# Kernel tuning notes

Hardware: AMD Instinct MI355X
Metric: run time of the kernel (lower is better)

## Reference

```python
import jax, jax.numpy as jnp
import numpy as np

N = 100000   # nodes
E = 1600000  # directed edges (avg degree 16)
IN, HID, OUT = 32, 64, 32


def setup_inputs() -> dict:
    key = jax.random.key(0)
    k0, k1, k2, k3 = jax.random.split(key, 4)
    x = jax.random.normal(k0, (N, IN), dtype=jnp.float32)
    edge_index = jax.random.randint(k1, (2, E), 0, N, dtype=jnp.int32)
    W1 = jax.random.normal(k2, (IN, HID), dtype=jnp.float32) * (1.0 / np.sqrt(IN))
    b1 = jnp.zeros((HID,), dtype=jnp.float32)
    W2 = jax.random.normal(k3, (HID, OUT), dtype=jnp.float32) * (1.0 / np.sqrt(HID))
    b2 = jnp.zeros((OUT,), dtype=jnp.float32)
    return {"x": x, "edge_index": edge_index, "W1": W1, "b1": b1, "W2": W2, "b2": b2}


def gcn_conv(x, src, dst, W, b, n):
    # GCNConv: D^{-1/2} (A + I) D^{-1/2} X W + b, deg computed after self-loops
    h = x @ W                                   # [N, d_out]
    ones = jnp.ones_like(dst, dtype=h.dtype)
    deg = jax.ops.segment_sum(ones, dst, num_segments=n)   # >= 1 (self-loops)
    dinv = jax.lax.rsqrt(jnp.maximum(deg, 1.0))
    norm = dinv[src] * dinv[dst]                # [E + N]
    agg = jax.ops.segment_sum(norm[:, None] * h[src], dst, num_segments=n)
    return agg + b


def reference(x, edge_index, W1, b1, W2, b2):
    n = x.shape[0]
    loop = jnp.arange(n, dtype=edge_index.dtype)
    src = jnp.concatenate([edge_index[0], loop])  # add self-loops once
    dst = jnp.concatenate([edge_index[1], loop])
    h = jax.nn.relu(gcn_conv(x, src, dst, W1, b1, n))
    # dropout omitted (eval mode)
    out = gcn_conv(h, src, dst, W2, b2, n)
    return out
```

## Files before the change

kernel.cpp:

```cpp
#include <hip/hip_runtime.h>
#include <stdint.h>

#define IN_F  32
#define HID_F 64
#define OUT_F 32

#define BKT_SHIFT 8
#define BKT_NODES 256
#define NBLK      512

__device__ inline unsigned short f2bf(float f) {
    unsigned u = __float_as_uint(f);
    return (unsigned short)((u + 0x7FFF + ((u >> 16) & 1)) >> 16);
}
__device__ inline float bflo(unsigned w) { return __uint_as_float(w << 16); }
__device__ inline float bfhi(unsigned w) { return __uint_as_float(w & 0xFFFF0000u); }

__global__ __launch_bounds__(256) void count_kernel(const int* __restrict__ dst,
                                                    int* __restrict__ cnt, int E, int nb)
{
    __shared__ int hist[1024];
    int tid = threadIdx.x;
    for (int i = tid; i < nb; i += 256) hist[i] = 0;
    __syncthreads();
    for (int e = blockIdx.x * 256 + tid; e < E; e += NBLK * 256)
        atomicAdd(&hist[dst[e] >> BKT_SHIFT], 1);
    __syncthreads();
    for (int i = tid; i < nb; i += 256) cnt[i * NBLK + blockIdx.x] = hist[i];
}

__global__ __launch_bounds__(NBLK) void bsum_kernel(const int* __restrict__ cnt,
                                                    int* __restrict__ bsum)
{
    __shared__ int s[NBLK];
    int tid = threadIdx.x, b = blockIdx.x;
    s[tid] = cnt[b * NBLK + tid];
    __syncthreads();
    for (int off = NBLK / 2; off > 0; off >>= 1) {
        if (tid < off) s[tid] += s[tid + off];
        __syncthreads();
    }
    if (tid == 0) bsum[b] = s[0];
}

__global__ __launch_bounds__(512) void bscan_kernel(int* __restrict__ bsum, int nb,
                                                    int* __restrict__ cellstart, int nc,
                                                    int* __restrict__ rowstart, int n, int E)
{
    __shared__ int s[512];
    int tid = threadIdx.x;
    int my = (tid < nb) ? bsum[tid] : 0;
    s[tid] = my;
    __syncthreads();
    for (int off = 1; off < 512; off <<= 1) {
        int t = (tid >= off) ? s[tid - off] : 0;
        __syncthreads();
        s[tid] += t;
        __syncthreads();
    }
    if (tid < nb) bsum[tid] = s[tid] - my;
    if (tid == 0) { cellstart[nc] = E; rowstart[n] = E; }
}

__global__ __launch_bounds__(NBLK) void cscan_kernel(const int* __restrict__ cnt,
                                                     const int* __restrict__ bsum,
                                                     int* __restrict__ cellstart)
{
    __shared__ int s[NBLK];
    int tid = threadIdx.x, b = blockIdx.x;
    int my = cnt[b * NBLK + tid];
    s[tid] = my;
    __syncthreads();
    for (int off = 1; off < NBLK; off <<= 1) {
        int t = (tid >= off) ? s[tid - off] : 0;
        __syncthreads();
        s[tid] += t;
        __syncthreads();
    }
    cellstart[b * NBLK + tid] = bsum[b] + s[tid] - my;
}

__global__ __launch_bounds__(256) void append_kernel(
    const int* __restrict__ src, const int* __restrict__ dst,
    const int* __restrict__ cellstart, unsigned* __restrict__ pairs, int E, int nb)
{
    __shared__ int cur[1024];
    int tid = threadIdx.x;
    for (int i = tid; i < nb; i += 256) cur[i] = cellstart[i * NBLK + blockIdx.x];
    __syncthreads();
    for (int e = blockIdx.x * 256 + tid; e < E; e += NBLK * 256) {
        int d = dst[e];
        int pos = atomicAdd(&cur[d >> BKT_SHIFT], 1);
        pairs[pos] = ((unsigned)src[e] << BKT_SHIFT) | (unsigned)(d & (BKT_NODES - 1));
    }
}

__global__ __launch_bounds__(256) void place_kernel(
    const int* __restrict__ cellstart, const unsigned* __restrict__ pairs,
    int* __restrict__ srcs, int* __restrict__ rowstart, float* __restrict__ dinv, int n)
{
    __shared__ int hist[BKT_NODES];
    __shared__ int ofs[BKT_NODES];
    int b = blockIdx.x, tid = threadIdx.x;
    int beg = cellstart[b * NBLK], end = cellstart[(b + 1) * NBLK];
    hist[tid] = 0;
    __syncthreads();
    for (int e = beg + tid; e < end; e += 256)
        atomicAdd(&hist[pairs[e] & (BKT_NODES - 1)], 1);
    __syncthreads();
    int my = hist[tid];
    ofs[tid] = my;
    __syncthreads();
    for (int off = 1; off < 256; off <<= 1) {
        int t = (tid >= off) ? ofs[tid - off] : 0;
        __syncthreads();
        ofs[tid] += t;
        __syncthreads();
    }
    int excl = ofs[tid] - my;
    int node = b * BKT_NODES + tid;
    if (node < n) {
        rowstart[node] = beg + excl;
        dinv[node] = rsqrtf((float)(my + 1));
    }
    __syncthreads();
    ofs[tid] = excl;
    __syncthreads();
    for (int e = beg + tid; e < end; e += 256) {
        unsigned p = pairs[e];
        int dl = p & (BKT_NODES - 1);
        int pos = beg + atomicAdd(&ofs[dl], 1);
        srcs[pos] = (int)(p >> BKT_SHIFT);
    }
}

__global__ void xs_kernel(const float* __restrict__ x, const float* __restrict__ dinv,
                          unsigned short* __restrict__ xsb, int n) {
    int t = blockIdx.x * blockDim.x + threadIdx.x;
    if (t < n * (IN_F / 4)) {
        float d = dinv[t >> 3];
        float4 v = ((const float4*)x)[t];
        ushort4 o;
        o.x = f2bf(v.x * d); o.y = f2bf(v.y * d);
        o.z = f2bf(v.z * d); o.w = f2bf(v.w * d);
        ((ushort4*)xsb)[t] = o;
    }
}

__global__ __launch_bounds__(512) void fused1_kernel(
    const int* __restrict__ rowstart, const int* __restrict__ srcs,
    const unsigned* __restrict__ xs2, const float* __restrict__ dinv,
    const float* __restrict__ b1, const float* __restrict__ W1,
    const float* __restrict__ W2, unsigned* __restrict__ hs2p, int n)
{
    __shared__ float W1s[IN_F * HID_F];
    __shared__ float W2s[HID_F * OUT_F];
    __shared__ float grow[32][IN_F + 1];
    __shared__ float hrow[32][HID_F + 1];
    int tid = threadIdx.x;
    for (int t = tid; t < IN_F * HID_F; t += 512) W1s[t] = W1[t];
    for (int t = tid; t < HID_F * OUT_F; t += 512) W2s[t] = W2[t];

    int nl = tid >> 4;
    unsigned q = tid & 15;
    int node = blockIdx.x * 32 + nl;
    bool active = node < n;
    int nodec = active ? node : 0;

    int beg = rowstart[nodec], end = active ? rowstart[nodec + 1] : beg;
    unsigned ws = active ? xs2[((unsigned)nodec << 4) + q] : 0u;
    float a0l = bflo(ws), a0h = bfhi(ws);
    float a1l = 0.f, a1h = 0.f, a2l = 0.f, a2h = 0.f, a3l = 0.f, a3h = 0.f;
    float a4l = 0.f, a4h = 0.f, a5l = 0.f, a5h = 0.f, a6l = 0.f, a6h = 0.f;
    float a7l = 0.f, a7h = 0.f;
    int e = beg;
    for (; e + 8 <= end; e += 8) {
        unsigned o0 = ((unsigned)srcs[e]     << 4) + q, o1 = ((unsigned)srcs[e + 1] << 4) + q;
        unsigned o2 = ((unsigned)srcs[e + 2] << 4) + q, o3 = ((unsigned)srcs[e + 3] << 4) + q;
        unsigned o4 = ((unsigned)srcs[e + 4] << 4) + q, o5 = ((unsigned)srcs[e + 5] << 4) + q;
        unsigned o6 = ((unsigned)srcs[e + 6] << 4) + q, o7 = ((unsigned)srcs[e + 7] << 4) + q;
        unsigned w0 = xs2[o0], w1 = xs2[o1], w2 = xs2[o2], w3 = xs2[o3];
        unsigned w4 = xs2[o4], w5 = xs2[o5], w6 = xs2[o6], w7 = xs2[o7];
        a0l += bflo(w0); a0h += bfhi(w0); a1l += bflo(w1); a1h += bfhi(w1);
        a2l += bflo(w2); a2h += bfhi(w2); a3l += bflo(w3); a3h += bfhi(w3);
        a4l += bflo(w4); a4h += bfhi(w4); a5l += bflo(w5); a5h += bfhi(w5);
        a6l += bflo(w6); a6h += bfhi(w6); a7l += bflo(w7); a7h += bfhi(w7);
    }
    for (; e + 4 <= end; e += 4) {
        unsigned o0 = ((unsigned)srcs[e]     << 4) + q, o1 = ((unsigned)srcs[e + 1] << 4) + q;
        unsigned o2 = ((unsigned)srcs[e + 2] << 4) + q, o3 = ((unsigned)srcs[e + 3] << 4) + q;
        unsigned w0 = xs2[o0], w1 = xs2[o1], w2 = xs2[o2], w3 = xs2[o3];
        a0l += bflo(w0); a0h += bfhi(w0); a1l += bflo(w1); a1h += bfhi(w1);
        a2l += bflo(w2); a2h += bfhi(w2); a3l += bflo(w3); a3h += bfhi(w3);
    }
    for (; e < end; ++e) {
        unsigned w0 = xs2[((unsigned)srcs[e] << 4) + q];
        a0l += bflo(w0); a0h += bfhi(w0);
    }
    float dv = dinv[nodec];
    grow[nl][2 * q]     = dv * (((a0l + a1l) + (a2l + a3l)) + ((a4l + a5l) + (a6l + a7l)));
    grow[nl][2 * q + 1] = dv * (((a0h + a1h) + (a2h + a3h)) + ((a4h + a5h) + (a6h + a7h)));
    __syncthreads();

    float h0 = b1[q], h1 = b1[q + 16], h2 = b1[q + 32], h3 = b1[q + 48];
    #pragma unroll
    for (int k = 0; k < IN_F; ++k) {
        float gk = grow[nl][k];
        h0 += gk * W1s[k * HID_F + q];
        h1 += gk * W1s[k * HID_F + q + 16];
        h2 += gk * W1s[k * HID_F + q + 32];
        h3 += gk * W1s[k * HID_F + q + 48];
    }
    hrow[nl][q]      = fmaxf(h0, 0.f);
    hrow[nl][q + 16] = fmaxf(h1, 0.f);
    hrow[nl][q + 32] = fmaxf(h2, 0.f);
    hrow[nl][q + 48] = fmaxf(h3, 0.f);
    __syncthreads();

    float p0 = 0.f, p1 = 0.f;
    #pragma unroll
    for (int k = 0; k < HID_F; ++k) {
        float hk = hrow[nl][k];
        p0 += hk * W2s[k * OUT_F + 2 * q];
        p1 += hk * W2s[k * OUT_F + 2 * q + 1];
    }
    if (active) {
        unsigned pack = (unsigned)f2bf(dv * p0) | ((unsigned)f2bf(dv * p1) << 16);
        hs2p[((unsigned)node << 4) + q] = pack;
    }
}

__global__ __launch_bounds__(256) void agg2_kernel(
    const int* __restrict__ rowstart, const int* __restrict__ srcs,
    const uint2* __restrict__ hs2p2, const float* __restrict__ dinv,
    const float* __restrict__ b2, float* __restrict__ out, int n)
{
    int t = blockIdx.x * blockDim.x + threadIdx.x;
    int node = t >> 3;
    if (node >= n) return;
    unsigned r = t & 7;
    int beg = rowstart[node], end = rowstart[node + 1];
    uint2 ws = hs2p2[((unsigned)node << 3) + r];
    float a0x = bflo(ws.x), a0y = bfhi(ws.x), a0z = bflo(ws.y), a0w = bfhi(ws.y);
    float a1x = 0.f, a1y = 0.f, a1z = 0.f, a1w = 0.f;
    float a2x = 0.f, a2y = 0.f, a2z = 0.f, a2w = 0.f;
    float a3x = 0.f, a3y = 0.f, a3z = 0.f, a3w = 0.f;
    int e = beg;
    for (; e + 4 <= end; e += 4) {
        unsigned o0 = ((unsigned)srcs[e]     << 3) + r, o1 = ((unsigned)srcs[e + 1] << 3) + r;
        unsigned o2 = ((unsigned)srcs[e + 2] << 3) + r, o3 = ((unsigned)srcs[e + 3] << 3) + r;
        uint2 w0 = hs2p2[o0], w1 = hs2p2[o1], w2 = hs2p2[o2], w3 = hs2p2[o3];
        a0x += bflo(w0.x); a0y += bfhi(w0.x); a0z += bflo(w0.y); a0w += bfhi(w0.y);
        a1x += bflo(w1.x); a1y += bfhi(w1.x); a1z += bflo(w1.y); a1w += bfhi(w1.y);
        a2x += bflo(w2.x); a2y += bfhi(w2.x); a2z += bflo(w2.y); a2w += bfhi(w2.y);
        a3x += bflo(w3.x); a3y += bfhi(w3.x); a3z += bflo(w3.y); a3w += bfhi(w3.y);
    }
    for (; e < end; ++e) {
        uint2 w0 = hs2p2[((unsigned)srcs[e] << 3) + r];
        a0x += bflo(w0.x); a0y += bfhi(w0.x); a0z += bflo(w0.y); a0w += bfhi(w0.y);
    }
    float dvv = dinv[node];
    float4 bb = ((const float4*)b2)[r];
    float4 res;
    res.x = dvv * ((a0x + a1x) + (a2x + a3x)) + bb.x;
    res.y = dvv * ((a0y + a1y) + (a2y + a3y)) + bb.y;
    res.z = dvv * ((a0z + a1z) + (a2z + a3z)) + bb.z;
    res.w = dvv * ((a0w + a1w) + (a2w + a3w)) + bb.w;
    ((float4*)out)[((size_t)node << 3) + r] = res;
}

extern "C" void kernel_launch(void* const* d_in, const int* in_sizes, int n_in,
                              void* d_out, int out_size, void* d_ws, size_t ws_size,
                              hipStream_t stream) {
    const float* x  = (const float*)d_in[0];
    const int*   ei = (const int*)  d_in[1];
    const float* W1 = (const float*)d_in[2];
    const float* b1 = (const float*)d_in[3];
    const float* W2 = (const float*)d_in[4];
    const float* b2 = (const float*)d_in[5];
    float* out = (float*)d_out;

    const int n = in_sizes[0] / IN_F;
    const int E = in_sizes[1] / 2;
    const int* src = ei;
    const int* dst = ei + E;

    const int nb = (n + BKT_NODES - 1) >> BKT_SHIFT;
    const int nc = nb * NBLK;

    auto align16 = [](int* p) { return (int*)(((uintptr_t)p + 15) & ~(uintptr_t)15); };
    int* ip = (int*)d_ws;
    int* cnt       = ip;                 ip += nc;
    int* cellstart = ip;                 ip += nc + 1;
    int* bsum      = ip;                 ip += nb + 1;
    int* rowstart  = ip;                 ip += n + 1;
    ip = align16(ip);
    unsigned* pairs = (unsigned*)ip;     ip += E;
    int* srcs_srt  = ip;                 ip += E;
    float* dinv = (float*)ip;            ip += n;
    ip = align16(ip);
    unsigned* xs2  = (unsigned*)ip;      ip += (size_t)n * IN_F / 2;
    ip = align16(ip);
    unsigned* hs2p = (unsigned*)ip;

    count_kernel<<<NBLK, 256, 0, stream>>>(dst, cnt, E, nb);
    bsum_kernel <<<nb, NBLK, 0, stream>>>(cnt, bsum);
    bscan_kernel<<<1, 512, 0, stream>>>(bsum, nb, cellstart, nc, rowstart, n, E);
    cscan_kernel<<<nb, NBLK, 0, stream>>>(cnt, bsum, cellstart);
    append_kernel<<<NBLK, 256, 0, stream>>>(src, dst, cellstart, pairs, E, nb);
    place_kernel<<<nb, 256, 0, stream>>>(cellstart, pairs, srcs_srt, rowstart, dinv, n);

    xs_kernel<<<((size_t)n * 8 + 255) / 256, 256, 0, stream>>>(x, dinv, (unsigned short*)xs2, n);

    fused1_kernel<<<(n + 31) / 32, 512, 0, stream>>>(rowstart, srcs_srt, xs2, dinv, b1, W1, W2, hs2p, n);
    agg2_kernel<<<((size_t)n * 8 + 255) / 256, 256, 0, stream>>>(rowstart, srcs_srt, (const uint2*)hs2p, dinv, b2, out, n);
}
```

Baseline: 214.5 us.

## Fuse bucket-sum into count and x scaling into place; add nontemporal loads and unrolling

Drops the bsum reduction kernel and instead has count_kernel accumulate per-bucket totals atomically after a memset. The x-scaling/bf16 pack kernel is folded into place_kernel, using per-bucket dinv held in shared memory. Streaming index reads and writes now use nontemporal loads and stores, and the gather loops in both aggregation kernels get a deeper unroll to keep more loads in flight. Together these remove two launches and make the edge-index streams bypass cache residency, in exchange for global atomics and more register pressure.

```diff
diff --git a/kernel.cpp b/kernel.cpp
--- a/kernel.cpp
+++ b/kernel.cpp
@@ -16,31 +16,25 @@
 __device__ inline float bflo(unsigned w) { return __uint_as_float(w << 16); }
 __device__ inline float bfhi(unsigned w) { return __uint_as_float(w & 0xFFFF0000u); }
 
+__device__ inline int ntld(const int* p) { return __builtin_nontemporal_load(p); }
+__device__ inline unsigned ntldu(const unsigned* p) { return __builtin_nontemporal_load(p); }
+
 __global__ __launch_bounds__(256) void count_kernel(const int* __restrict__ dst,
-                                                    int* __restrict__ cnt, int E, int nb)
+                                                    int* __restrict__ cnt,
+                                                    int* __restrict__ bsum, int E, int nb)
 {
     __shared__ int hist[1024];
     int tid = threadIdx.x;
     for (int i = tid; i < nb; i += 256) hist[i] = 0;
     __syncthreads();
     for (int e = blockIdx.x * 256 + tid; e < E; e += NBLK * 256)
-        atomicAdd(&hist[dst[e] >> BKT_SHIFT], 1);
-    __syncthreads();
-    for (int i = tid; i < nb; i += 256) cnt[i * NBLK + blockIdx.x] = hist[i];
-}
-
-__global__ __launch_bounds__(NBLK) void bsum_kernel(const int* __restrict__ cnt,
-                                                    int* __restrict__ bsum)
-{
-    __shared__ int s[NBLK];
-    int tid = threadIdx.x, b = blockIdx.x;
-    s[tid] = cnt[b * NBLK + tid];
-    __syncthreads();
-    for (int off = NBLK / 2; off > 0; off >>= 1) {
-        if (tid < off) s[tid] += s[tid + off];
-        __syncthreads();
-    }
-    if (tid == 0) bsum[b] = s[0];
+        atomicAdd(&hist[ntld(&dst[e]) >> BKT_SHIFT], 1);
+    __syncthreads();
+    for (int i = tid; i < nb; i += 256) {
+        int h = hist[i];
+        cnt[i * NBLK + blockIdx.x] = h;
+        if (h) atomicAdd(&bsum[i], h);
+    }
 }
 
 __global__ __launch_bounds__(512) void bscan_kernel(int* __restrict__ bsum, int nb,
@@ -89,24 +83,28 @@
     for (int i = tid; i < nb; i += 256) cur[i] = cellstart[i * NBLK + blockIdx.x];
     __syncthreads();
     for (int e = blockIdx.x * 256 + tid; e < E; e += NBLK * 256) {
-        int d = dst[e];
+        int d = ntld(&dst[e]);
+        int s = ntld(&src[e]);
         int pos = atomicAdd(&cur[d >> BKT_SHIFT], 1);
-        pairs[pos] = ((unsigned)src[e] << BKT_SHIFT) | (unsigned)(d & (BKT_NODES - 1));
+        __builtin_nontemporal_store(((unsigned)s << BKT_SHIFT) | (unsigned)(d & (BKT_NODES - 1)),
+                                    &pairs[pos]);
     }
 }
 
 __global__ __launch_bounds__(256) void place_kernel(
     const int* __restrict__ cellstart, const unsigned* __restrict__ pairs,
-    int* __restrict__ srcs, int* __restrict__ rowstart, float* __restrict__ dinv, int n)
+    int* __restrict__ srcs, int* __restrict__ rowstart, float* __restrict__ dinv,
+    const float* __restrict__ x, unsigned* __restrict__ xs2, int n)
 {
     __shared__ int hist[BKT_NODES];
     __shared__ int ofs[BKT_NODES];
+    __shared__ float sdv[BKT_NODES];
     int b = blockIdx.x, tid = threadIdx.x;
     int beg = cellstart[b * NBLK], end = cellstart[(b + 1) * NBLK];
     hist[tid] = 0;
     __syncthreads();
     for (int e = beg + tid; e < end; e += 256)
-        atomicAdd(&hist[pairs[e] & (BKT_NODES - 1)], 1);
+        atomicAdd(&hist[ntldu(&pairs[e]) & (BKT_NODES - 1)], 1);
     __syncthreads();
     int my = hist[tid];
     ofs[tid] = my;
@@ -119,31 +117,32 @@
     }
     int excl = ofs[tid] - my;
     int node = b * BKT_NODES + tid;
+    float dv = rsqrtf((float)(my + 1));
+    sdv[tid] = dv;
     if (node < n) {
         rowstart[node] = beg + excl;
-        dinv[node] = rsqrtf((float)(my + 1));
+        dinv[node] = dv;
     }
     __syncthreads();
     ofs[tid] = excl;
     __syncthreads();
     for (int e = beg + tid; e < end; e += 256) {
-        unsigned p = pairs[e];
+        unsigned p = ntldu(&pairs[e]);
         int dl = p & (BKT_NODES - 1);
         int pos = beg + atomicAdd(&ofs[dl], 1);
         srcs[pos] = (int)(p >> BKT_SHIFT);
     }
-}
-
-__global__ void xs_kernel(const float* __restrict__ x, const float* __restrict__ dinv,
-                          unsigned short* __restrict__ xsb, int n) {
-    int t = blockIdx.x * blockDim.x + threadIdx.x;
-    if (t < n * (IN_F / 4)) {
-        float d = dinv[t >> 3];
-        float4 v = ((const float4*)x)[t];
-        ushort4 o;
-        o.x = f2bf(v.x * d); o.y = f2bf(v.y * d);
-        o.z = f2bf(v.z * d); o.w = f2bf(v.w * d);
-        ((ushort4*)xsb)[t] = o;
+    int base = b * BKT_NODES;
+    for (int idx = tid; idx < BKT_NODES * (IN_F / 2); idx += 256) {
+        int nl = idx >> 4;
+        int p  = idx & 15;
+        int nd = base + nl;
+        if (nd < n) {
+            float2 v = ((const float2*)x)[((size_t)nd << 4) + p];
+            float d = sdv[nl];
+            unsigned pack = (unsigned)f2bf(v.x * d) | ((unsigned)f2bf(v.y * d) << 16);
+            xs2[((size_t)nd << 4) + p] = pack;
+        }
     }
 }
 
@@ -174,11 +173,33 @@
     float a4l = 0.f, a4h = 0.f, a5l = 0.f, a5h = 0.f, a6l = 0.f, a6h = 0.f;
     float a7l = 0.f, a7h = 0.f;
     int e = beg;
+    for (; e + 16 <= end; e += 16) {
+        unsigned o0 = ((unsigned)ntld(&srcs[e])      << 4) + q, o1 = ((unsigned)ntld(&srcs[e + 1]) << 4) + q;
+        unsigned o2 = ((unsigned)ntld(&srcs[e + 2])  << 4) + q, o3 = ((unsigned)ntld(&srcs[e + 3]) << 4) + q;
+        unsigned o4 = ((unsigned)ntld(&srcs[e + 4])  << 4) + q, o5 = ((unsigned)ntld(&srcs[e + 5]) << 4) + q;
+        unsigned o6 = ((unsigned)ntld(&srcs[e + 6])  << 4) + q, o7 = ((unsigned)ntld(&srcs[e + 7]) << 4) + q;
+        unsigned o8 = ((unsigned)ntld(&srcs[e + 8])  << 4) + q, o9 = ((unsigned)ntld(&srcs[e + 9]) << 4) + q;
+        unsigned oa = ((unsigned)ntld(&srcs[e + 10]) << 4) + q, ob = ((unsigned)ntld(&srcs[e + 11]) << 4) + q;
+        unsigned oc = ((unsigned)ntld(&srcs[e + 12]) << 4) + q, od = ((unsigned)ntld(&srcs[e + 13]) << 4) + q;
+        unsigned oe = ((unsigned)ntld(&srcs[e + 14]) << 4) + q, of_ = ((unsigned)ntld(&srcs[e + 15]) << 4) + q;
+        unsigned w0 = xs2[o0], w1 = xs2[o1], w2 = xs2[o2], w3 = xs2[o3];
+        unsigned w4 = xs2[o4], w5 = xs2[o5], w6 = xs2[o6], w7 = xs2[o7];
+        unsigned w8 = xs2[o8], w9 = xs2[o9], wa = xs2[oa], wb = xs2[ob];
+        unsigned wc = xs2[oc], wd = xs2[od], we = xs2[oe], wf = xs2[of_];
+        a0l += bflo(w0); a0h += bfhi(w0); a1l += bflo(w1); a1h += bfhi(w1);
+        a2l += bflo(w2); a2h += bfhi(w2); a3l += bflo(w3); a3h += bfhi(w3);
+        a4l += bflo(w4); a4h += bfhi(w4); a5l += bflo(w5); a5h += bfhi(w5);
+        a6l += bflo(w6); a6h += bfhi(w6); a7l += bflo(w7); a7h += bfhi(w7);
+        a0l += bflo(w8); a0h += bfhi(w8); a1l += bflo(w9); a1h += bfhi(w9);
+        a2l += bflo(wa); a2h += bfhi(wa); a3l += bflo(wb); a3h += bfhi(wb);
+        a4l += bflo(wc); a4h += bfhi(wc); a5l += bflo(wd); a5h += bfhi(wd);
+        a6l += bflo(we); a6h += bfhi(we); a7l += bflo(wf); a7h += bfhi(wf);
+    }
     for (; e + 8 <= end; e += 8) {
-        unsigned o0 = ((unsigned)srcs[e]     << 4) + q, o1 = ((unsigned)srcs[e + 1] << 4) + q;
-        unsigned o2 = ((unsigned)srcs[e + 2] << 4) + q, o3 = ((unsigned)srcs[e + 3] << 4) + q;
-        unsigned o4 = ((unsigned)srcs[e + 4] << 4) + q, o5 = ((unsigned)srcs[e + 5] << 4) + q;
-        unsigned o6 = ((unsigned)srcs[e + 6] << 4) + q, o7 = ((unsigned)srcs[e + 7] << 4) + q;
+        unsigned o0 = ((unsigned)ntld(&srcs[e])     << 4) + q, o1 = ((unsigned)ntld(&srcs[e + 1]) << 4) + q;
+        unsigned o2 = ((unsigned)ntld(&srcs[e + 2]) << 4) + q, o3 = ((unsigned)ntld(&srcs[e + 3]) << 4) + q;
+        unsigned o4 = ((unsigned)ntld(&srcs[e + 4]) << 4) + q, o5 = ((unsigned)ntld(&srcs[e + 5]) << 4) + q;
+        unsigned o6 = ((unsigned)ntld(&srcs[e + 6]) << 4) + q, o7 = ((unsigned)ntld(&srcs[e + 7]) << 4) + q;
         unsigned w0 = xs2[o0], w1 = xs2[o1], w2 = xs2[o2], w3 = xs2[o3];
         unsigned w4 = xs2[o4], w5 = xs2[o5], w6 = xs2[o6], w7 = xs2[o7];
         a0l += bflo(w0); a0h += bfhi(w0); a1l += bflo(w1); a1h += bfhi(w1);
@@ -187,14 +208,14 @@
         a6l += bflo(w6); a6h += bfhi(w6); a7l += bflo(w7); a7h += bfhi(w7);
     }
     for (; e + 4 <= end; e += 4) {
-        unsigned o0 = ((unsigned)srcs[e]     << 4) + q, o1 = ((unsigned)srcs[e + 1] << 4) + q;
-        unsigned o2 = ((unsigned)srcs[e + 2] << 4) + q, o3 = ((unsigned)srcs[e + 3] << 4) + q;
+        unsigned o0 = ((unsigned)ntld(&srcs[e])     << 4) + q, o1 = ((unsigned)ntld(&srcs[e + 1]) << 4) + q;
+        unsigned o2 = ((unsigned)ntld(&srcs[e + 2]) << 4) + q, o3 = ((unsigned)ntld(&srcs[e + 3]) << 4) + q;
         unsigned w0 = xs2[o0], w1 = xs2[o1], w2 = xs2[o2], w3 = xs2[o3];
         a0l += bflo(w0); a0h += bfhi(w0); a1l += bflo(w1); a1h += bfhi(w1);
         a2l += bflo(w2); a2h += bfhi(w2); a3l += bflo(w3); a3h += bfhi(w3);
     }
     for (; e < end; ++e) {
-        unsigned w0 = xs2[((unsigned)srcs[e] << 4) + q];
+        unsigned w0 = xs2[((unsigned)ntld(&srcs[e]) << 4) + q];
         a0l += bflo(w0); a0h += bfhi(w0);
     }
     float dv = dinv[nodec];
@@ -246,9 +267,25 @@
     float a2x = 0.f, a2y = 0.f, a2z = 0.f, a2w = 0.f;
     float a3x = 0.f, a3y = 0.f, a3z = 0.f, a3w = 0.f;
     int e = beg;
+    for (; e + 8 <= end; e += 8) {
+        unsigned o0 = ((unsigned)ntld(&srcs[e])     << 3) + r, o1 = ((unsigned)ntld(&srcs[e + 1]) << 3) + r;
+        unsigned o2 = ((unsigned)ntld(&srcs[e + 2]) << 3) + r, o3 = ((unsigned)ntld(&srcs[e + 3]) << 3) + r;
+        unsigned o4 = ((unsigned)ntld(&srcs[e + 4]) << 3) + r, o5 = ((unsigned)ntld(&srcs[e + 5]) << 3) + r;
+        unsigned o6 = ((unsigned)ntld(&srcs[e + 6]) << 3) + r, o7 = ((unsigned)ntld(&srcs[e + 7]) << 3) + r;
+        uint2 w0 = hs2p2[o0], w1 = hs2p2[o1], w2 = hs2p2[o2], w3 = hs2p2[o3];
+        uint2 w4 = hs2p2[o4], w5 = hs2p2[o5], w6 = hs2p2[o6], w7 = hs2p2[o7];
+        a0x += bflo(w0.x); a0y += bfhi(w0.x); a0z += bflo(w0.y); a0w += bfhi(w0.y);
+        a1x += bflo(w1.x); a1y += bfhi(w1.x); a1z += bflo(w1.y); a1w += bfhi(w1.y);
+        a2x += bflo(w2.x); a2y += bfhi(w2.x); a2z += bflo(w2.y); a2w += bfhi(w2.y);
+        a3x += bflo(w3.x); a3y += bfhi(w3.x); a3z += bflo(w3.y); a3w += bfhi(w3.y);
+        a0x += bflo(w4.x); a0y += bfhi(w4.x); a0z += bflo(w4.y); a0w += bfhi(w4.y);
+        a1x += bflo(w5.x); a1y += bfhi(w5.x); a1z += bflo(w5.y); a1w += bfhi(w5.y);
+        a2x += bflo(w6.x); a2y += bfhi(w6.x); a2z += bflo(w6.y); a2w += bfhi(w6.y);
+        a3x += bflo(w7.x); a3y += bfhi(w7.x); a3z += bflo(w7.y); a3w += bfhi(w7.y);
+    }
     for (; e + 4 <= end; e += 4) {
-        unsigned o0 = ((unsigned)srcs[e]     << 3) + r, o1 = ((unsigned)srcs[e + 1] << 3) + r;
-        unsigned o2 = ((unsigned)srcs[e + 2] << 3) + r, o3 = ((unsigned)srcs[e + 3] << 3) + r;
+        unsigned o0 = ((unsigned)ntld(&srcs[e])     << 3) + r, o1 = ((unsigned)ntld(&srcs[e + 1]) << 3) + r;
+        unsigned o2 = ((unsigned)ntld(&srcs[e + 2]) << 3) + r, o3 = ((unsigned)ntld(&srcs[e + 3]) << 3) + r;
         uint2 w0 = hs2p2[o0], w1 = hs2p2[o1], w2 = hs2p2[o2], w3 = hs2p2[o3];
         a0x += bflo(w0.x); a0y += bfhi(w0.x); a0z += bflo(w0.y); a0w += bfhi(w0.y);
         a1x += bflo(w1.x); a1y += bfhi(w1.x); a1z += bflo(w1.y); a1w += bfhi(w1.y);
@@ -256,7 +293,7 @@
         a3x += bflo(w3.x); a3y += bfhi(w3.x); a3z += bflo(w3.y); a3w += bfhi(w3.y);
     }
     for (; e < end; ++e) {
-        uint2 w0 = hs2p2[((unsigned)srcs[e] << 3) + r];
+        uint2 w0 = hs2p2[((unsigned)ntld(&srcs[e]) << 3) + r];
         a0x += bflo(w0.x); a0y += bfhi(w0.x); a0z += bflo(w0.y); a0w += bfhi(w0.y);
     }
     float dvv = dinv[node];
@@ -303,14 +340,12 @@
     ip = align16(ip);
     unsigned* hs2p = (unsigned*)ip;
 
-    count_kernel<<<NBLK, 256, 0, stream>>>(dst, cnt, E, nb);
-    bsum_kernel <<<nb, NBLK, 0, stream>>>(cnt, bsum);
+    hipMemsetAsync(bsum, 0, (nb + 1) * sizeof(int), stream);
+    count_kernel<<<NBLK, 256, 0, stream>>>(dst, cnt, bsum, E, nb);
     bscan_kernel<<<1, 512, 0, stream>>>(bsum, nb, cellstart, nc, rowstart, n, E);
     cscan_kernel<<<nb, NBLK, 0, stream>>>(cnt, bsum, cellstart);
     append_kernel<<<NBLK, 256, 0, stream>>>(src, dst, cellstart, pairs, E, nb);
-    place_kernel<<<nb, 256, 0, stream>>>(cellstart, pairs, srcs_srt, rowstart, dinv, n);
-
-    xs_kernel<<<((size_t)n * 8 + 255) / 256, 256, 0, stream>>>(x, dinv, (unsigned short*)xs2, n);
+    place_kernel<<<nb, 256, 0, stream>>>(cellstart, pairs, srcs_srt, rowstart, dinv, x, xs2, n);
 
     fused1_kernel<<<(n + 31) / 32, 512, 0, stream>>>(rowstart, srcs_srt, xs2, dinv, b1, W1, W2, hs2p, n);
     agg2_kernel<<<((size_t)n * 8 + 255) / 256, 256, 0, stream>>>(rowstart, srcs_srt, (const uint2*)hs2p, dinv, b2, out, n);
```

Result: slower. 264.8 us (+23.4%).
